# Kernel tuning notes

Measured on AMD Instinct MI355X. Metric: run time of the kernel, lower is better.

The kernel has to match this reference:

```python
import jax, jax.numpy as jnp
import numpy as np

SCALE_FACTOR = 1.0
VIS_MAX = 1024


def setup_inputs() -> dict:
    key = jax.random.key(0)
    kq, kk, kv = jax.random.split(key, 3)
    B, C, H, W = 4, 256, 64, 64
    Q = jax.random.normal(kq, (B, C, H, W), dtype=jnp.float32)
    K = jax.random.normal(kk, (B, C, H, W), dtype=jnp.float32)
    V = jax.random.normal(kv, (B, C, H, W), dtype=jnp.float32)
    return {"Q": Q, "K": K, "V": V}


def reference(Q, K, V):
    # Q,K: [B,C,H,W] -> flatten spatial dims to HW
    B, C, H, W = Q.shape
    HW = H * W
    Q_flat = Q.reshape(B, C, HW).transpose(0, 2, 1)  # [B, HW, C]
    K_flat = K.reshape(B, C, HW)                      # [B, C, HW]
    # Full scaled score matrix [B, HW, HW]; argmax over keys reproduces the
    # chunked running-max/argmax (strict '>' update keeps first max, matching
    # jnp.argmax tie-breaking).
    S = jnp.einsum('bqc,bck->bqk', Q_flat, K_flat) * SCALE_FACTOR
    H_idx = jnp.argmax(S, axis=2).astype(jnp.int64)   # [B, HW]
    vis = min(VIS_MAX, HW)
    S_vis = S[:, :vis, :vis]                          # [B, vis, vis]
    return S_vis, H_idx
```

## Files before the change

### kernel.cpp

```cpp
#include <hip/hip_runtime.h>
#include <stdint.h>

#define B_   4
#define C_   256
#define HW_  4096
#define VIS_ 1024
#define KE_  768

using half8   = __attribute__((ext_vector_type(8))) _Float16;
using floatx4 = __attribute__((ext_vector_type(4))) float;

__device__ __forceinline__ unsigned mapf(float v) {
    unsigned u = __float_as_uint(v);
    return (u & 0x80000000u) ? ~u : (u | 0x80000000u);
}

__global__ void init_ws_kernel(unsigned long long* ws, int n) {
    int i = blockIdx.x * blockDim.x + threadIdx.x;
    if (i < n) ws[i] = 0ull;
}

__global__ void finalize_kernel(const unsigned long long* __restrict__ ws,
                                float* __restrict__ out1, int n) {
    int i = blockIdx.x * blockDim.x + threadIdx.x;
    if (i < n) {
        unsigned kinv = (unsigned)(ws[i] & 0xFFFFFFFFull);
        out1[i] = (float)(HW_ - 1 - (int)kinv);
    }
}


__global__ __launch_bounds__(256) void split_transpose_kernel(
    const float* __restrict__ Q, const float* __restrict__ K,
    _Float16* __restrict__ Aexp, _Float16* __restrict__ Bexp)
{
    __shared__ float tile[64][65];
    const int hw0 = blockIdx.x * 64;
    const int c0  = blockIdx.y * 64;
    const int z = blockIdx.z, b = z >> 1, which = z & 1;
    const float* src = (which ? K : Q) + (size_t)b * C_ * HW_;
    _Float16* dst = (which ? Bexp : Aexp) + (size_t)b * HW_ * KE_;
    const int t = threadIdx.x;

    #pragma unroll
    for (int i = 0; i < 4; ++i) {
        int c  = (t >> 4) + i * 16;
        int hw = (t & 15) * 4;
        float4 v = *(const float4*)(src + (size_t)(c0 + c) * HW_ + hw0 + hw);
        tile[c][hw] = v.x; tile[c][hw+1] = v.y; tile[c][hw+2] = v.z; tile[c][hw+3] = v.w;
    }
    __syncthreads();

    #pragma unroll
    for (int i = 0; i < 2; ++i) {
        int id  = t + i * 256;
        int row = id >> 3;
        int c8  = (id & 7) * 8;
        half8 h8, l8;
        #pragma unroll
        for (int j = 0; j < 8; ++j) {
            float v = tile[c8 + j][row];
            _Float16 h = (_Float16)v;
            h8[j] = h;
            l8[j] = (_Float16)(v - (float)h);
        }
        _Float16* base = dst + (size_t)(hw0 + row) * KE_ + c0 + c8;
        *(half8*)(base + 0 * C_) = h8;
        *(half8*)(base + 1 * C_) = which ? l8 : h8;
        *(half8*)(base + 2 * C_) = which ? h8 : l8;
    }
}

__device__ __forceinline__ void gl2lds16(const _Float16* g, _Float16* l) {
    __builtin_amdgcn_global_load_lds(
        (const __attribute__((address_space(1))) void*)g,
        (__attribute__((address_space(3))) void*)l, 16, 0, 0);
}


#define BARRIER __builtin_amdgcn_s_barrier()
#define LGKM0   asm volatile("s_waitcnt lgkmcnt(0)" ::: "memory")
#define VMC(n)  asm volatile("s_waitcnt vmcnt(" #n ")" ::: "memory")
#define SCHEDB  __builtin_amdgcn_sched_barrier(0)

__device__ __forceinline__ void stage_half(const _Float16* __restrict__ g,
                                           _Float16* lb, int t, int kbase)
{
    #pragma unroll
    for (int j = 0; j < 2; ++j) {
        const int c   = t + j * 512;
        const int row = c >> 2;
        const int ch  = (c & 3) ^ ((row >> 1) & 3);
        gl2lds16(g + (size_t)row * KE_ + kbase + ch * 8, lb + c * 8);
    }
}

template<int DB, int KH, int MQ>
__device__ __forceinline__ void ds_load_a(const _Float16* lds, int wave_m, int s,
                                          int quad, half8 (&a)[4]) {
    const _Float16* base = lds + (DB * 4 + KH) * 8192;
    #pragma unroll
    for (int mi = 0; mi < 4; ++mi) {
        int row = wave_m * 128 + MQ * 64 + mi * 16 + s;
        int ch  = quad ^ ((row >> 1) & 3);
        a[mi] = *(const half8*)(base + row * 32 + ch * 8);
    }
}

template<int DB, int KH>
__device__ __forceinline__ void ds_load_b(const _Float16* lds, int wave_n, int s,
                                          int quad, half8 (&bfr)[4]) {
    const _Float16* base = lds + (DB * 4 + 2 + KH) * 8192;
    #pragma unroll
    for (int ni = 0; ni < 4; ++ni) {
        int col = wave_n * 64 + ni * 16 + s;
        int ch  = quad ^ ((col >> 1) & 3);
        bfr[ni] = *(const half8*)(base + col * 32 + ch * 8);
    }
}

template<int MQ>
__device__ __forceinline__ void do_mfma(const half8 (&a)[4], const half8 (&bfr)[4],
                                        floatx4 (&acc)[8][4]) {
    __builtin_amdgcn_s_setprio(1);
    #pragma unroll
    for (int mi = 0; mi < 4; ++mi)
        #pragma unroll
        for (int ni = 0; ni < 4; ++ni)
            acc[MQ * 4 + mi][ni] = __builtin_amdgcn_mfma_f32_16x16x32_f16(
                a[mi], bfr[ni], acc[MQ * 4 + mi][ni], 0, 0, 0);
    __builtin_amdgcn_s_setprio(0);
}

__global__ __launch_bounds__(512, 1) void gemm_mfma_kernel(
    const _Float16* __restrict__ Aexp, const _Float16* __restrict__ Bexp,
    float* __restrict__ out0, unsigned long long* __restrict__ keys)
{
    __shared__ __align__(16) _Float16 lds[65536];

    const int t      = threadIdx.x;
    const int lane   = t & 63;
    const int wave   = t >> 6;
    const int quad   = lane >> 4;
    const int s      = lane & 15;
    const int wave_m = wave >> 2;
    const int wave_n = wave & 3;
    const int kt = blockIdx.x, qt = blockIdx.y, b = blockIdx.z;

    const _Float16* Agl = Aexp + (size_t)b * HW_ * KE_ + (size_t)(qt * 256) * KE_;
    const _Float16* Bgl = Bexp + (size_t)b * HW_ * KE_ + (size_t)(kt * 256) * KE_;

    stage_half(Agl, lds + 0 * 8192, t, 0);
    stage_half(Bgl, lds + 2 * 8192, t, 0);
    stage_half(Agl, lds + 1 * 8192, t, 32);
    stage_half(Bgl, lds + 3 * 8192, t, 32);
    stage_half(Agl, lds + 4 * 8192, t, 64);
    stage_half(Bgl, lds + 6 * 8192, t, 64);
    VMC(4);
    BARRIER; SCHEDB;

    half8 a[4], bfr[4];
    floatx4 acc[8][4] = {};

    #pragma unroll 1
    for (int it = 0; it < 5; ++it) {
        const int kb1 = (2 * it + 1) * 64;
        const int kb2 = kb1 + 64;
        const int kb3 = kb1 + 128;
        ds_load_a<0, 0, 0>(lds, wave_m, s, quad, a);
        ds_load_b<0, 0>(lds, wave_n, s, quad, bfr);
        stage_half(Agl, lds + 5 * 8192, t, kb1 + 32);
        BARRIER; LGKM0;
        do_mfma<0>(a, bfr, acc);
        BARRIER;
        ds_load_a<0, 0, 1>(lds, wave_m, s, quad, a);
        stage_half(Bgl, lds + 7 * 8192, t, kb1 + 32);
        BARRIER; LGKM0;
        do_mfma<1>(a, bfr, acc);
        BARRIER;
        ds_load_a<0, 1, 0>(lds, wave_m, s, quad, a);
        ds_load_b<0, 1>(lds, wave_n, s, quad, bfr);
        stage_half(Agl, lds + 0 * 8192, t, kb2);
        BARRIER; LGKM0;
        do_mfma<0>(a, bfr, acc);
        BARRIER;
        ds_load_a<0, 1, 1>(lds, wave_m, s, quad, a);
        stage_half(Bgl, lds + 2 * 8192, t, kb2);
        BARRIER; LGKM0;
        do_mfma<1>(a, bfr, acc);
        VMC(4);
        BARRIER; SCHEDB;
        ds_load_a<1, 0, 0>(lds, wave_m, s, quad, a);
        ds_load_b<1, 0>(lds, wave_n, s, quad, bfr);
        stage_half(Agl, lds + 1 * 8192, t, kb2 + 32);
        BARRIER; LGKM0;
        do_mfma<0>(a, bfr, acc);
        BARRIER;
        ds_load_a<1, 0, 1>(lds, wave_m, s, quad, a);
        stage_half(Bgl, lds + 3 * 8192, t, kb2 + 32);
        BARRIER; LGKM0;
        do_mfma<1>(a, bfr, acc);
        BARRIER;
        ds_load_a<1, 1, 0>(lds, wave_m, s, quad, a);
        ds_load_b<1, 1>(lds, wave_n, s, quad, bfr);
        stage_half(Agl, lds + 4 * 8192, t, kb3);
        BARRIER; LGKM0;
        do_mfma<0>(a, bfr, acc);
        BARRIER;
        ds_load_a<1, 1, 1>(lds, wave_m, s, quad, a);
        stage_half(Bgl, lds + 6 * 8192, t, kb3);
        BARRIER; LGKM0;
        do_mfma<1>(a, bfr, acc);
        VMC(4);
        BARRIER; SCHEDB;
    }

    stage_half(Agl, lds + 5 * 8192, t, 736);
    stage_half(Bgl, lds + 7 * 8192, t, 736);
    VMC(0);
    __syncthreads();

    ds_load_a<0, 0, 0>(lds, wave_m, s, quad, a);
    ds_load_b<0, 0>(lds, wave_n, s, quad, bfr);
    do_mfma<0>(a, bfr, acc);
    ds_load_a<0, 0, 1>(lds, wave_m, s, quad, a);
    do_mfma<1>(a, bfr, acc);
    ds_load_a<0, 1, 0>(lds, wave_m, s, quad, a);
    ds_load_b<0, 1>(lds, wave_n, s, quad, bfr);
    do_mfma<0>(a, bfr, acc);
    ds_load_a<0, 1, 1>(lds, wave_m, s, quad, a);
    do_mfma<1>(a, bfr, acc);
    ds_load_a<1, 0, 0>(lds, wave_m, s, quad, a);
    ds_load_b<1, 0>(lds, wave_n, s, quad, bfr);
    do_mfma<0>(a, bfr, acc);
    ds_load_a<1, 0, 1>(lds, wave_m, s, quad, a);
    do_mfma<1>(a, bfr, acc);
    ds_load_a<1, 1, 0>(lds, wave_m, s, quad, a);
    ds_load_b<1, 1>(lds, wave_n, s, quad, bfr);
    do_mfma<0>(a, bfr, acc);
    ds_load_a<1, 1, 1>(lds, wave_m, s, quad, a);
    do_mfma<1>(a, bfr, acc);

    if (qt < 4 && kt < 4) {
        #pragma unroll
        for (int mi8 = 0; mi8 < 8; ++mi8)
            #pragma unroll
            for (int r = 0; r < 4; ++r) {
                int grow = qt * 256 + wave_m * 128 + mi8 * 16 + quad * 4 + r;
                float* orow = out0 + ((size_t)b * VIS_ + grow) * VIS_ + kt * 256 + wave_n * 64;
                #pragma unroll
                for (int ni = 0; ni < 4; ++ni)
                    orow[ni * 16 + s] = acc[mi8][ni][r];
            }
    }

    __syncthreads();
    unsigned long long* red = (unsigned long long*)lds;

    #pragma unroll
    for (int mi8 = 0; mi8 < 8; ++mi8) {
        #pragma unroll
        for (int r = 0; r < 4; ++r) {
            float best = acc[mi8][0][r];
            int bcol = wave_n * 64 + s;
            #pragma unroll
            for (int ni = 1; ni < 4; ++ni) {
                float v = acc[mi8][ni][r];
                if (v > best) { best = v; bcol = wave_n * 64 + ni * 16 + s; }
            }
            int gcol = kt * 256 + bcol;
            unsigned long long key = ((unsigned long long)mapf(best) << 32)
                                   | (unsigned)(HW_ - 1 - gcol);
            #pragma unroll
            for (int m = 1; m < 16; m <<= 1) {
                unsigned long long o = __shfl_xor(key, m, 64);
                if (o > key) key = o;
            }
            if (s == 0)
                red[(wave_m * 128 + mi8 * 16 + quad * 4 + r) * 4 + wave_n] = key;
        }
    }
    __syncthreads();
    if (t < 256) {
        const unsigned long long* rr = red + t * 4;
        unsigned long long k0 = rr[0], k1 = rr[1], k2 = rr[2], k3 = rr[3];
        unsigned long long m01 = k0 > k1 ? k0 : k1;
        unsigned long long m23 = k2 > k3 ? k2 : k3;
        atomicMax(&keys[(size_t)b * HW_ + qt * 256 + t], m01 > m23 ? m01 : m23);
    }
}

#define BT   64
#define BK   32
#define LDP  68

__global__ __launch_bounds__(256) void gemm_argmax_kernel(
    const float* __restrict__ Q, const float* __restrict__ K,
    float* __restrict__ out0, unsigned long long* __restrict__ ws)
{
    __shared__ float As[BK][LDP];
    __shared__ float Bs[BK][LDP];
    __shared__ unsigned long long red[BT][17];

    const int t  = threadIdx.x;
    const int tx = t & 15;
    const int ty = t >> 4;
    const int k0 = blockIdx.x * BT;
    const int q0 = blockIdx.y * BT;
    const int b  = blockIdx.z;

    const float* Qb = Q + (size_t)b * C_ * HW_;
    const float* Kb = K + (size_t)b * C_ * HW_;

    float acc[4][4] = {{0.f},{0.f},{0.f},{0.f}};

    for (int c0 = 0; c0 < C_; c0 += BK) {
        #pragma unroll
        for (int i = 0; i < 2; ++i) {
            int idx = i * 256 + t;
            int row = idx >> 4;
            int col = (idx & 15) * 4;
            const float4 a  = *(const float4*)(Qb + (size_t)(c0 + row) * HW_ + q0 + col);
            const float4 bv = *(const float4*)(Kb + (size_t)(c0 + row) * HW_ + k0 + col);
            *(float4*)(&As[row][col]) = a;
            *(float4*)(&Bs[row][col]) = bv;
        }
        __syncthreads();
        #pragma unroll
        for (int cc = 0; cc < BK; ++cc) {
            const float4 av = *(const float4*)(&As[cc][ty * 4]);
            const float4 bv = *(const float4*)(&Bs[cc][tx * 4]);
            const float a_[4] = {av.x, av.y, av.z, av.w};
            const float b_[4] = {bv.x, bv.y, bv.z, bv.w};
            #pragma unroll
            for (int i = 0; i < 4; ++i)
                #pragma unroll
                for (int j = 0; j < 4; ++j)
                    acc[i][j] = fmaf(a_[i], b_[j], acc[i][j]);
        }
        __syncthreads();
    }

    if (q0 < VIS_ && k0 < VIS_) {
        #pragma unroll
        for (int i = 0; i < 4; ++i) {
            float4 v = make_float4(acc[i][0], acc[i][1], acc[i][2], acc[i][3]);
            size_t off = (size_t)b * VIS_ * VIS_ + (size_t)(q0 + ty * 4 + i) * VIS_ + (k0 + tx * 4);
            *(float4*)(out0 + off) = v;
        }
    }

    #pragma unroll
    for (int i = 0; i < 4; ++i) {
        float best = acc[i][0];
        int   bj   = 0;
        #pragma unroll
        for (int j = 1; j < 4; ++j)
            if (acc[i][j] > best) { best = acc[i][j]; bj = j; }
        int kidx = k0 + tx * 4 + bj;
        unsigned long long key = ((unsigned long long)mapf(best) << 32)
                               | (unsigned)(HW_ - 1 - kidx);
        red[ty * 4 + i][tx] = key;
    }
    __syncthreads();
    if (t < BT) {
        unsigned long long best = red[t][0];
        #pragma unroll
        for (int j = 1; j < 16; ++j) {
            unsigned long long v = red[t][j];
            if (v > best) best = v;
        }
        atomicMax(&ws[(size_t)b * HW_ + q0 + t], best);
    }
}

extern "C" void kernel_launch(void* const* d_in, const int* in_sizes, int n_in,
                              void* d_out, int out_size, void* d_ws, size_t ws_size,
                              hipStream_t stream) {
    const float* Q = (const float*)d_in[0];
    const float* K = (const float*)d_in[1];
    float* out0 = (float*)d_out;
    float* out1 = out0 + (size_t)B_ * VIS_ * VIS_;

    unsigned long long* keys = (unsigned long long*)d_ws;
    const size_t keys_bytes = (size_t)B_ * HW_ * 8;
    const size_t exp_elems  = (size_t)B_ * HW_ * KE_;
    const size_t need = keys_bytes + 2 * exp_elems * sizeof(_Float16);

    const int n = B_ * HW_;
    init_ws_kernel<<<(n + 255) / 256, 256, 0, stream>>>(keys, n);

    if (ws_size >= need) {
        _Float16* Aexp = (_Float16*)((char*)d_ws + keys_bytes);
        _Float16* Bexp = Aexp + exp_elems;
        split_transpose_kernel<<<dim3(HW_ / 64, C_ / 64, 2 * B_), 256, 0, stream>>>(Q, K, Aexp, Bexp);
        gemm_mfma_kernel<<<dim3(HW_ / 256, HW_ / 256, B_), 512, 0, stream>>>(Aexp, Bexp, out0, keys);
    } else {
        gemm_argmax_kernel<<<dim3(HW_ / BT, HW_ / BT, B_), 256, 0, stream>>>(Q, K, out0, keys);
    }

    finalize_kernel<<<(n + 255) / 256, 256, 0, stream>>>(keys, out1, n);
}
```

Baseline: 224.3 us.

## Run the GEMM as one block per tile that walks all batches with a continuous pipeline

The MFMA GEMM grid drops from 16x16x4 to 16x16 blocks. Each block now loops over all four batches as one 48-step k-pipeline, so prefetching runs across batch boundaries. The per-batch store and argmax epilogue runs inside the loop while the next batch's tiles are already loading, and the accumulators are then reset. Zeroing of the argmax keys moves into the transpose kernel, which removes a separate launch. This targets the pipeline fill and drain bubbles, the multi-wave tail and launch overhead. The cost is an extra 8 KB of LDS per block and less parallelism if there are fewer CUs than blocks.

```diff
diff --git a/kernel.cpp b/kernel.cpp
--- a/kernel.cpp
+++ b/kernel.cpp
@@ -6,6 +6,7 @@
 #define HW_  4096
 #define VIS_ 1024
 #define KE_  768
+#define NT_  48
 
 using half8   = __attribute__((ext_vector_type(8))) _Float16;
 using floatx4 = __attribute__((ext_vector_type(4))) float;
@@ -32,15 +33,19 @@
 
 __global__ __launch_bounds__(256) void split_transpose_kernel(
     const float* __restrict__ Q, const float* __restrict__ K,
-    _Float16* __restrict__ Aexp, _Float16* __restrict__ Bexp)
+    _Float16* __restrict__ Aexp, _Float16* __restrict__ Bexp,
+    unsigned long long* __restrict__ keys)
 {
     __shared__ float tile[64][65];
+    const int t = threadIdx.x;
+    if (blockIdx.y == 0 && blockIdx.z == 0)
+        keys[blockIdx.x * 256 + t] = 0ull;
+
     const int hw0 = blockIdx.x * 64;
     const int c0  = blockIdx.y * 64;
     const int z = blockIdx.z, b = z >> 1, which = z & 1;
     const float* src = (which ? K : Q) + (size_t)b * C_ * HW_;
     _Float16* dst = (which ? Bexp : Aexp) + (size_t)b * HW_ * KE_;
-    const int t = threadIdx.x;
 
     #pragma unroll
     for (int i = 0; i < 4; ++i) {
@@ -84,14 +89,14 @@
 #define SCHEDB  __builtin_amdgcn_sched_barrier(0)
 
 __device__ __forceinline__ void stage_half(const _Float16* __restrict__ g,
-                                           _Float16* lb, int t, int kbase)
+                                           _Float16* lb, int t)
 {
     #pragma unroll
     for (int j = 0; j < 2; ++j) {
         const int c   = t + j * 512;
         const int row = c >> 2;
         const int ch  = (c & 3) ^ ((row >> 1) & 3);
-        gl2lds16(g + (size_t)row * KE_ + kbase + ch * 8, lb + c * 8);
+        gl2lds16(g + (size_t)row * KE_ + ch * 8, lb + c * 8);
     }
 }
 
@@ -137,6 +142,7 @@
     float* __restrict__ out0, unsigned long long* __restrict__ keys)
 {
     __shared__ __align__(16) _Float16 lds[65536];
+    __shared__ unsigned long long red[256][4];
 
     const int t      = threadIdx.x;
     const int lane   = t & 63;
@@ -145,17 +151,27 @@
     const int s      = lane & 15;
     const int wave_m = wave >> 2;
     const int wave_n = wave & 3;
-    const int kt = blockIdx.x, qt = blockIdx.y, b = blockIdx.z;
-
-    const _Float16* Agl = Aexp + (size_t)b * HW_ * KE_ + (size_t)(qt * 256) * KE_;
-    const _Float16* Bgl = Bexp + (size_t)b * HW_ * KE_ + (size_t)(kt * 256) * KE_;
-
-    stage_half(Agl, lds + 0 * 8192, t, 0);
-    stage_half(Bgl, lds + 2 * 8192, t, 0);
-    stage_half(Agl, lds + 1 * 8192, t, 32);
-    stage_half(Bgl, lds + 3 * 8192, t, 32);
-    stage_half(Agl, lds + 4 * 8192, t, 64);
-    stage_half(Bgl, lds + 6 * 8192, t, 64);
+    const int kt = blockIdx.x, qt = blockIdx.y;
+
+    const size_t bstr = (size_t)HW_ * KE_;
+    const _Float16* Aq = Aexp + (size_t)(qt * 256) * KE_;
+    const _Float16* Bk = Bexp + (size_t)(kt * 256) * KE_;
+
+    auto APTR = [&](int Tk) -> const _Float16* {
+        if (Tk > NT_ - 1) Tk = NT_ - 1;
+        return Aq + (size_t)(Tk / 12) * bstr + (Tk % 12) * 64;
+    };
+    auto BPTR = [&](int Tk) -> const _Float16* {
+        if (Tk > NT_ - 1) Tk = NT_ - 1;
+        return Bk + (size_t)(Tk / 12) * bstr + (Tk % 12) * 64;
+    };
+
+    stage_half(APTR(0),      lds + 0 * 8192, t);
+    stage_half(BPTR(0),      lds + 2 * 8192, t);
+    stage_half(APTR(0) + 32, lds + 1 * 8192, t);
+    stage_half(BPTR(0) + 32, lds + 3 * 8192, t);
+    stage_half(APTR(1),      lds + 4 * 8192, t);
+    stage_half(BPTR(1),      lds + 6 * 8192, t);
     VMC(4);
     BARRIER; SCHEDB;
 
@@ -163,131 +179,116 @@
     floatx4 acc[8][4] = {};
 
     #pragma unroll 1
-    for (int it = 0; it < 5; ++it) {
-        const int kb1 = (2 * it + 1) * 64;
-        const int kb2 = kb1 + 64;
-        const int kb3 = kb1 + 128;
+    for (int j = 0; j < NT_ / 2; ++j) {
+        const int T = 2 * j;
+        const _Float16* a1 = APTR(T + 1); const _Float16* b1 = BPTR(T + 1);
+        const _Float16* a2 = APTR(T + 2); const _Float16* b2 = BPTR(T + 2);
+        const _Float16* a3 = APTR(T + 3); const _Float16* b3 = BPTR(T + 3);
+
         ds_load_a<0, 0, 0>(lds, wave_m, s, quad, a);
         ds_load_b<0, 0>(lds, wave_n, s, quad, bfr);
-        stage_half(Agl, lds + 5 * 8192, t, kb1 + 32);
+        stage_half(a1 + 32, lds + 5 * 8192, t);
         BARRIER; LGKM0;
         do_mfma<0>(a, bfr, acc);
         BARRIER;
         ds_load_a<0, 0, 1>(lds, wave_m, s, quad, a);
-        stage_half(Bgl, lds + 7 * 8192, t, kb1 + 32);
+        stage_half(b1 + 32, lds + 7 * 8192, t);
         BARRIER; LGKM0;
         do_mfma<1>(a, bfr, acc);
         BARRIER;
         ds_load_a<0, 1, 0>(lds, wave_m, s, quad, a);
         ds_load_b<0, 1>(lds, wave_n, s, quad, bfr);
-        stage_half(Agl, lds + 0 * 8192, t, kb2);
+        stage_half(a2, lds + 0 * 8192, t);
         BARRIER; LGKM0;
         do_mfma<0>(a, bfr, acc);
         BARRIER;
         ds_load_a<0, 1, 1>(lds, wave_m, s, quad, a);
-        stage_half(Bgl, lds + 2 * 8192, t, kb2);
+        stage_half(b2, lds + 2 * 8192, t);
         BARRIER; LGKM0;
         do_mfma<1>(a, bfr, acc);
         VMC(4);
         BARRIER; SCHEDB;
         ds_load_a<1, 0, 0>(lds, wave_m, s, quad, a);
         ds_load_b<1, 0>(lds, wave_n, s, quad, bfr);
-        stage_half(Agl, lds + 1 * 8192, t, kb2 + 32);
+        stage_half(a2 + 32, lds + 1 * 8192, t);
         BARRIER; LGKM0;
         do_mfma<0>(a, bfr, acc);
         BARRIER;
         ds_load_a<1, 0, 1>(lds, wave_m, s, quad, a);
-        stage_half(Bgl, lds + 3 * 8192, t, kb2 + 32);
+        stage_half(b2 + 32, lds + 3 * 8192, t);
         BARRIER; LGKM0;
         do_mfma<1>(a, bfr, acc);
         BARRIER;
         ds_load_a<1, 1, 0>(lds, wave_m, s, quad, a);
         ds_load_b<1, 1>(lds, wave_n, s, quad, bfr);
-        stage_half(Agl, lds + 4 * 8192, t, kb3);
+        stage_half(a3, lds + 4 * 8192, t);
         BARRIER; LGKM0;
         do_mfma<0>(a, bfr, acc);
         BARRIER;
         ds_load_a<1, 1, 1>(lds, wave_m, s, quad, a);
-        stage_half(Bgl, lds + 6 * 8192, t, kb3);
+        stage_half(b3, lds + 6 * 8192, t);
         BARRIER; LGKM0;
         do_mfma<1>(a, bfr, acc);
         VMC(4);
         BARRIER; SCHEDB;
-    }
-
-    stage_half(Agl, lds + 5 * 8192, t, 736);
-    stage_half(Bgl, lds + 7 * 8192, t, 736);
-    VMC(0);
-    __syncthreads();
-
-    ds_load_a<0, 0, 0>(lds, wave_m, s, quad, a);
-    ds_load_b<0, 0>(lds, wave_n, s, quad, bfr);
-    do_mfma<0>(a, bfr, acc);
-    ds_load_a<0, 0, 1>(lds, wave_m, s, quad, a);
-    do_mfma<1>(a, bfr, acc);
-    ds_load_a<0, 1, 0>(lds, wave_m, s, quad, a);
-    ds_load_b<0, 1>(lds, wave_n, s, quad, bfr);
-    do_mfma<0>(a, bfr, acc);
-    ds_load_a<0, 1, 1>(lds, wave_m, s, quad, a);
-    do_mfma<1>(a, bfr, acc);
-    ds_load_a<1, 0, 0>(lds, wave_m, s, quad, a);
-    ds_load_b<1, 0>(lds, wave_n, s, quad, bfr);
-    do_mfma<0>(a, bfr, acc);
-    ds_load_a<1, 0, 1>(lds, wave_m, s, quad, a);
-    do_mfma<1>(a, bfr, acc);
-    ds_load_a<1, 1, 0>(lds, wave_m, s, quad, a);
-    ds_load_b<1, 1>(lds, wave_n, s, quad, bfr);
-    do_mfma<0>(a, bfr, acc);
-    ds_load_a<1, 1, 1>(lds, wave_m, s, quad, a);
-    do_mfma<1>(a, bfr, acc);
-
-    if (qt < 4 && kt < 4) {
-        #pragma unroll
-        for (int mi8 = 0; mi8 < 8; ++mi8)
+
+        if ((T % 12) == 10) {
+            const int bq = T / 12;
+
+            if (qt < 4 && kt < 4) {
+                #pragma unroll
+                for (int mi8 = 0; mi8 < 8; ++mi8)
+                    #pragma unroll
+                    for (int r = 0; r < 4; ++r) {
+                        int grow = qt * 256 + wave_m * 128 + mi8 * 16 + quad * 4 + r;
+                        float* orow = out0 + ((size_t)bq * VIS_ + grow) * VIS_
+                                    + kt * 256 + wave_n * 64;
+                        #pragma unroll
+                        for (int ni = 0; ni < 4; ++ni)
+                            orow[ni * 16 + s] = acc[mi8][ni][r];
+                    }
+            }
+
             #pragma unroll
-            for (int r = 0; r < 4; ++r) {
-                int grow = qt * 256 + wave_m * 128 + mi8 * 16 + quad * 4 + r;
-                float* orow = out0 + ((size_t)b * VIS_ + grow) * VIS_ + kt * 256 + wave_n * 64;
+            for (int mi8 = 0; mi8 < 8; ++mi8) {
+                #pragma unroll
+                for (int r = 0; r < 4; ++r) {
+                    float best = acc[mi8][0][r];
+                    int bcol = wave_n * 64 + s;
+                    #pragma unroll
+                    for (int ni = 1; ni < 4; ++ni) {
+                        float v = acc[mi8][ni][r];
+                        if (v > best) { best = v; bcol = wave_n * 64 + ni * 16 + s; }
+                    }
+                    int gcol = kt * 256 + bcol;
+                    unsigned long long key = ((unsigned long long)mapf(best) << 32)
+                                           | (unsigned)(HW_ - 1 - gcol);
+                    #pragma unroll
+                    for (int m = 1; m < 16; m <<= 1) {
+                        unsigned long long o = __shfl_xor(key, m, 64);
+                        if (o > key) key = o;
+                    }
+                    if (s == 0)
+                        red[wave_m * 128 + mi8 * 16 + quad * 4 + r][wave & 3] = key;
+                }
+            }
+            LGKM0; BARRIER;
+            if (t < 256) {
+                const unsigned long long* rr = red[t];
+                unsigned long long k0 = rr[0], k1 = rr[1], k2 = rr[2], k3 = rr[3];
+                unsigned long long m01 = k0 > k1 ? k0 : k1;
+                unsigned long long m23 = k2 > k3 ? k2 : k3;
+                atomicMax(&keys[(size_t)bq * HW_ + qt * 256 + t], m01 > m23 ? m01 : m23);
+            }
+            #pragma unroll
+            for (int mi8 = 0; mi8 < 8; ++mi8)
                 #pragma unroll
                 for (int ni = 0; ni < 4; ++ni)
-                    orow[ni * 16 + s] = acc[mi8][ni][r];
-            }
-    }
-
-    __syncthreads();
-    unsigned long long* red = (unsigned long long*)lds;
-
-    #pragma unroll
-    for (int mi8 = 0; mi8 < 8; ++mi8) {
-        #pragma unroll
-        for (int r = 0; r < 4; ++r) {
-            float best = acc[mi8][0][r];
-            int bcol = wave_n * 64 + s;
-            #pragma unroll
-            for (int ni = 1; ni < 4; ++ni) {
-                float v = acc[mi8][ni][r];
-                if (v > best) { best = v; bcol = wave_n * 64 + ni * 16 + s; }
-            }
-            int gcol = kt * 256 + bcol;
-            unsigned long long key = ((unsigned long long)mapf(best) << 32)
-                                   | (unsigned)(HW_ - 1 - gcol);
-            #pragma unroll
-            for (int m = 1; m < 16; m <<= 1) {
-                unsigned long long o = __shfl_xor(key, m, 64);
-                if (o > key) key = o;
-            }
-            if (s == 0)
-                red[(wave_m * 128 + mi8 * 16 + quad * 4 + r) * 4 + wave_n] = key;
-        }
-    }
-    __syncthreads();
-    if (t < 256) {
-        const unsigned long long* rr = red + t * 4;
-        unsigned long long k0 = rr[0], k1 = rr[1], k2 = rr[2], k3 = rr[3];
-        unsigned long long m01 = k0 > k1 ? k0 : k1;
-        unsigned long long m23 = k2 > k3 ? k2 : k3;
-        atomicMax(&keys[(size_t)b * HW_ + qt * 256 + t], m01 > m23 ? m01 : m23);
-    }
+                    acc[mi8][ni] = (floatx4){0.f, 0.f, 0.f, 0.f};
+        }
+    }
+
+    VMC(0);
 }
 
 #define BT   64
@@ -388,14 +389,14 @@
     const size_t need = keys_bytes + 2 * exp_elems * sizeof(_Float16);
 
     const int n = B_ * HW_;
-    init_ws_kernel<<<(n + 255) / 256, 256, 0, stream>>>(keys, n);
 
     if (ws_size >= need) {
         _Float16* Aexp = (_Float16*)((char*)d_ws + keys_bytes);
         _Float16* Bexp = Aexp + exp_elems;
-        split_transpose_kernel<<<dim3(HW_ / 64, C_ / 64, 2 * B_), 256, 0, stream>>>(Q, K, Aexp, Bexp);
-        gemm_mfma_kernel<<<dim3(HW_ / 256, HW_ / 256, B_), 512, 0, stream>>>(Aexp, Bexp, out0, keys);
+        split_transpose_kernel<<<dim3(HW_ / 64, C_ / 64, 2 * B_), 256, 0, stream>>>(Q, K, Aexp, Bexp, keys);
+        gemm_mfma_kernel<<<dim3(HW_ / 256, HW_ / 256), 512, 0, stream>>>(Aexp, Bexp, out0, keys);
     } else {
+        init_ws_kernel<<<(n + 255) / 256, 256, 0, stream>>>(keys, n);
         gemm_argmax_kernel<<<dim3(HW_ / BT, HW_ / BT, B_), 256, 0, stream>>>(Q, K, out0, keys);
     }
 
```

Measured after the change: 261.3 us. 1.16x slower.
